# Optimization experiments

Measured on AMD Instinct MI355X. Metric: run time of the kernel, lower is better.

The kernel has to match this reference:

```python
import jax, jax.numpy as jnp
import numpy as np

EMBED_DIM = 1024
NUM_HEADS = 16
HEAD_DIM = EMBED_DIM // NUM_HEADS
SCALING = HEAD_DIM ** -0.5


def setup_inputs() -> dict:
    key = jax.random.key(0)
    ks = jax.random.split(key, 10)
    B, S, D = 2, 2048, EMBED_DIM
    lim = 1.0 / np.sqrt(D)  # torch Linear default init scale
    def lin(k):
        kw, kb = jax.random.split(k)
        W = jax.random.uniform(kw, (D, D), jnp.float32, -lim, lim)
        b = jax.random.uniform(kb, (D,), jnp.float32, -lim, lim)
        return W, b
    Wq, bq = lin(ks[0])
    Wk, bk = lin(ks[1])
    Wv, bv = lin(ks[2])
    Wo, bo = lin(ks[3])
    hidden_states = jax.random.normal(ks[4], (B, S, D), jnp.float32)
    attention_mask = jnp.ones((B, S), jnp.int32)  # unused by the module's forward
    return {"hidden_states": hidden_states, "attention_mask": attention_mask,
            "Wq": Wq, "bq": bq, "Wk": Wk, "bk": bk, "Wv": Wv, "bv": bv,
            "Wo": Wo, "bo": bo}


def reference(hidden_states, attention_mask, Wq, bq, Wk, bk, Wv, bv, Wo, bo):
    B, S, D = hidden_states.shape
    H, hd = NUM_HEADS, HEAD_DIM

    def split_heads(x):  # [B,S,D] -> [B,H,S,hd]
        return x.reshape(B, S, H, hd).transpose(0, 2, 1, 3)

    q = split_heads(hidden_states @ Wq.T + bq) * SCALING
    k = split_heads(hidden_states @ Wk.T + bk)
    v = split_heads(hidden_states @ Wv.T + bv)

    scores = jnp.einsum("bhqd,bhkd->bhqk", q, k)  # [B,H,S,S]
    mask_value = jnp.finfo(scores.dtype).min
    causal = jnp.triu(jnp.ones((S, S), bool), k=1)  # True above diagonal
    scores = jnp.where(causal, mask_value, scores)
    probs = jax.nn.softmax(scores, axis=-1)

    out = jnp.einsum("bhqk,bhkd->bhqd", probs, v)  # [B,H,S,hd]
    out = out.transpose(0, 2, 1, 3).reshape(B, S, D)
    return out @ Wo.T + bo
```

## Files before the change

### kernel.cpp

```cpp
#include <hip/hip_runtime.h>


typedef __bf16 bf16;
typedef __attribute__((ext_vector_type(8))) __bf16 bf16x8;
typedef __attribute__((ext_vector_type(4))) __bf16 bf16x4;
typedef __attribute__((ext_vector_type(4))) float f32x4;

#define MFMA16(a, b, c) __builtin_amdgcn_mfma_f32_16x16x32_bf16((a), (b), (c), 0, 0, 0)

__device__ __forceinline__ void gl_lds16(const bf16* g, bf16* l) {
  __builtin_amdgcn_global_load_lds(
      (__attribute__((address_space(1))) void*)g,
      (__attribute__((address_space(3))) void*)l, 16, 0, 0);
}

__global__ __launch_bounds__(256) void cvt5(
    const float* __restrict__ x, const float* __restrict__ wq,
    const float* __restrict__ wk, const float* __restrict__ wv,
    const float* __restrict__ wo,
    bf16* __restrict__ xb, bf16* __restrict__ wqb, bf16* __restrict__ wkb,
    bf16* __restrict__ wvb, bf16* __restrict__ wob) {
  const int bx = blockIdx.x;
  const float* s;
  bf16* d;
  int base;
  if (bx < 4096)      { s = x;  d = xb;  base = bx; }
  else if (bx < 5120) { s = wq; d = wqb; base = bx - 4096; }
  else if (bx < 6144) { s = wk; d = wkb; base = bx - 5120; }
  else if (bx < 7168) { s = wv; d = wvb; base = bx - 6144; }
  else                { s = wo; d = wob; base = bx - 7168; }
  const int i = base * 1024 + threadIdx.x * 4;
  const float4 v = *(const float4*)(s + i);
  bf16x4 o;
  o[0] = (bf16)v.x; o[1] = (bf16)v.y; o[2] = (bf16)v.z; o[3] = (bf16)v.w;
  *(bf16x4*)(d + i) = o;
}

__global__ __launch_bounds__(256) void vtrans(const bf16* __restrict__ v,
                                              bf16* __restrict__ vt) {
  __shared__ bf16 Ts[64 * 80];
  const int t = threadIdx.x;
  const int st = blockIdx.x;
  const int bh = blockIdx.y;
  const int bb = bh >> 4, h = bh & 15;
  const bf16* src = v + ((size_t)bb * 2048 + st * 64) * 1024 + h * 64;
#pragma unroll
  for (int i = 0; i < 2; ++i) {
    const int idx = i * 256 + t;
    const int sl = idx >> 3, c = idx & 7;
    *(bf16x8*)&Ts[sl * 80 + c * 8] = *(const bf16x8*)(src + (size_t)sl * 1024 + c * 8);
  }
  __syncthreads();
  bf16* dst = vt + (size_t)bh * 64 * 2048 + st * 64;
#pragma unroll
  for (int i = 0; i < 2; ++i) {
    const int idx = i * 256 + t;
    const int d = idx >> 3, c2 = idx & 7;
    bf16x8 tmp;
#pragma unroll
    for (int e = 0; e < 8; ++e) tmp[e] = Ts[(c2 * 8 + e) * 80 + d];
    *(bf16x8*)(dst + (size_t)d * 2048 + c2 * 8) = tmp;
  }
}

template <int BM, typename OutT>
__global__ __launch_bounds__(256, 2) void gemm_bt3(
    const bf16* __restrict__ A,
    const bf16* __restrict__ W0, const bf16* __restrict__ W1, const bf16* __restrict__ W2,
    const float* __restrict__ B0, const float* __restrict__ B1, const float* __restrict__ B2,
    OutT* __restrict__ O0, OutT* __restrict__ O1, OutT* __restrict__ O2,
    float s0, float s1, float s2, int K) {
  constexpr int WM = BM / 32;
  __shared__ bf16 As[BM * 64];
  __shared__ bf16 Bs[128 * 64];

  const int t = threadIdx.x;
  const int lane = t & 63;
  const int wv = t >> 6;
  const int wm = wv & 1, wn = wv >> 1;
  const int qd = lane >> 4, ln = lane & 15;

  const int which = blockIdx.x >> 3;
  const bf16* W = (which == 0) ? W0 : (which == 1) ? W1 : W2;
  const float* Bi = (which == 0) ? B0 : (which == 1) ? B1 : B2;
  OutT* O = (which == 0) ? O0 : (which == 1) ? O1 : O2;
  const float scale = (which == 0) ? s0 : (which == 1) ? s1 : s2;

  const int n0 = (blockIdx.x & 7) * 128;
  const int m0 = blockIdx.y * BM;

  f32x4 acc[WM][4] = {};

  for (int k0 = 0; k0 < K; k0 += 64) {
#pragma unroll
    for (int i = 0; i < BM / 32; ++i) {
      const int s = i * 256 + t;
      const int row = s >> 3;
      const int c = (s & 7) ^ (row & 7);
      gl_lds16(A + (size_t)(m0 + row) * K + k0 + c * 8, &As[s * 8]);
    }
#pragma unroll
    for (int i = 0; i < 4; ++i) {
      const int s = i * 256 + t;
      const int row = s >> 3;
      const int c = (s & 7) ^ (row & 7);
      gl_lds16(W + (size_t)(n0 + row) * K + k0 + c * 8, &Bs[s * 8]);
    }
    __syncthreads();

#pragma unroll
    for (int ks = 0; ks < 2; ++ks) {
      bf16x8 af[WM], bw[4];
#pragma unroll
      for (int i = 0; i < WM; ++i) {
        const int r = wm * (BM / 2) + i * 16 + ln;
        af[i] = *(const bf16x8*)&As[r * 64 + (((ks * 4 + qd) ^ (ln & 7)) << 3)];
      }
#pragma unroll
      for (int j = 0; j < 4; ++j) {
        const int r = wn * 64 + j * 16 + ln;
        bw[j] = *(const bf16x8*)&Bs[r * 64 + (((ks * 4 + qd) ^ (ln & 7)) << 3)];
      }
#pragma unroll
      for (int i = 0; i < WM; ++i)
#pragma unroll
        for (int j = 0; j < 4; ++j)
          acc[i][j] = MFMA16(af[i], bw[j], acc[i][j]);
    }
    __syncthreads();
  }

#pragma unroll
  for (int i = 0; i < WM; ++i) {
    const int row = m0 + wm * (BM / 2) + i * 16 + qd * 4;
#pragma unroll
    for (int j = 0; j < 4; ++j) {
      const int col = n0 + wn * 64 + j * 16 + ln;
      const float bias = Bi[col];
#pragma unroll
      for (int r = 0; r < 4; ++r) {
        const float v = (acc[i][j][r] + bias) * scale;
        O[(size_t)(row + r) * 1024 + col] = (OutT)v;
      }
    }
  }
}

__global__ __launch_bounds__(256, 4) void attn_causal(
    const bf16* __restrict__ Q, const bf16* __restrict__ Kg,
    const bf16* __restrict__ VT, bf16* __restrict__ Ob) {
  __shared__ bf16 Ks[2][64 * 64];
  __shared__ bf16 Vts[2][64 * 64];
  __shared__ bf16 Ps[4][16 * 64];

  const int t = threadIdx.x;
  const int lane = t & 63;
  const int w = t >> 6;
  const int qd = lane >> 4, ln = lane & 15;

  const int blk = blockIdx.x;
  const int bh = blk & 31;
  const int g = blk >> 5;
  const int a = g & 7, b = g >> 3;
  const int tq = (b == 0) ? (31 - a) : (b == 1) ? (16 + a) : (b == 2) ? (15 - a) : a;
  const int bb = bh >> 4, h = bh & 15;
  const size_t rowbase = (size_t)bb * 2048;
  const bf16* vtb = VT + (size_t)bh * 64 * 2048;

  const int q0 = tq * 64;
  const int nj = tq + 1;

  auto stage = [&](int buf, int j) {
    const bf16* kp = Kg + (rowbase + j * 64) * 1024 + h * 64;
#pragma unroll
    for (int i = 0; i < 2; ++i) {
      const int s = i * 256 + t;
      const int kv = s >> 3;
      const int c = (s & 7) ^ (kv & 7);
      gl_lds16(kp + (size_t)kv * 1024 + c * 8, &Ks[buf][s * 8]);
    }
#pragma unroll
    for (int i = 0; i < 2; ++i) {
      const int s = i * 256 + t;
      const int d = s >> 3;
      const int c = (s & 7) ^ (d & 7);
      gl_lds16(vtb + (size_t)d * 2048 + j * 64 + c * 8, &Vts[buf][s * 8]);
    }
  };

  const bf16* qp = Q + (rowbase + q0 + w * 16) * 1024 + h * 64;
  bf16x8 qf[2];
#pragma unroll
  for (int ks = 0; ks < 2; ++ks)
    qf[ks] = *(const bf16x8*)(qp + (size_t)ln * 1024 + ks * 32 + qd * 8);

  float l_run[4] = {0.f, 0.f, 0.f, 0.f};
  f32x4 accO[4] = {};

  stage(0, 0);

#pragma unroll 1
  for (int j = 0; j < nj; ++j) {
    const int buf = j & 1;
    __syncthreads();
    if (j + 1 < nj) stage(buf ^ 1, j + 1);

    f32x4 accS[4] = {};
#pragma unroll
    for (int ks = 0; ks < 2; ++ks) {
#pragma unroll
      for (int nt = 0; nt < 4; ++nt) {
        const bf16x8 bk = *(const bf16x8*)
            &Ks[buf][(nt * 16 + ln) * 64 + (((ks * 4 + qd) ^ (ln & 7)) << 3)];
        accS[nt] = MFMA16(qf[ks], bk, accS[nt]);
      }
    }

    if (j == nj - 1) {
#pragma unroll
      for (int r = 0; r < 4; ++r) {
        const int row = qd * 4 + r;
        const int qg = q0 + w * 16 + row;
        float sum = 0.f;
#pragma unroll
        for (int nt = 0; nt < 4; ++nt) {
          float p = __expf(accS[nt][r]);
          const int col = nt * 16 + ln;
          if ((j * 64 + col) > qg) p = 0.f;
          sum += p;
          Ps[w][row * 64 + ((((col >> 3) ^ (row & 7))) << 3) + (col & 7)] = (bf16)p;
        }
        l_run[r] += sum;
      }
    } else {
#pragma unroll
      for (int r = 0; r < 4; ++r) {
        const int row = qd * 4 + r;
        float sum = 0.f;
#pragma unroll
        for (int nt = 0; nt < 4; ++nt) {
          const float p = __expf(accS[nt][r]);
          const int col = nt * 16 + ln;
          sum += p;
          Ps[w][row * 64 + ((((col >> 3) ^ (row & 7))) << 3) + (col & 7)] = (bf16)p;
        }
        l_run[r] += sum;
      }
    }

#pragma unroll
    for (int kt = 0; kt < 2; ++kt) {
      const bf16x8 ap = *(const bf16x8*)
          &Ps[w][ln * 64 + (((kt * 4 + qd) ^ (ln & 7)) << 3)];
#pragma unroll
      for (int nt = 0; nt < 4; ++nt) {
        const bf16x8 bv = *(const bf16x8*)
            &Vts[buf][(nt * 16 + ln) * 64 + (((kt * 4 + qd) ^ (ln & 7)) << 3)];
        accO[nt] = MFMA16(ap, bv, accO[nt]);
      }
    }
  }

  bf16* op = Ob + (rowbase + q0 + w * 16) * 1024 + h * 64;
#pragma unroll
  for (int r = 0; r < 4; ++r) {
    float l = l_run[r];
#pragma unroll
    for (int off = 1; off < 16; off <<= 1) l += __shfl_xor(l, off, 64);
    const float inv_l = 1.0f / l;
#pragma unroll
    for (int nt = 0; nt < 4; ++nt)
      op[(size_t)(qd * 4 + r) * 1024 + nt * 16 + ln] = (bf16)(accO[nt][r] * inv_l);
  }
}

extern "C" void kernel_launch(void* const* d_in, const int* in_sizes, int n_in,
                              void* d_out, int out_size, void* d_ws, size_t ws_size,
                              hipStream_t stream) {
  const float* X  = (const float*)d_in[0];
  const float* Wq = (const float*)d_in[2];
  const float* bq = (const float*)d_in[3];
  const float* Wk = (const float*)d_in[4];
  const float* bk = (const float*)d_in[5];
  const float* Wv = (const float*)d_in[6];
  const float* bv = (const float*)d_in[7];
  const float* Wo = (const float*)d_in[8];
  const float* bo = (const float*)d_in[9];
  float* out = (float*)d_out;

  bf16* xb  = (bf16*)d_ws;
  bf16* wqb = xb  + (size_t)4096 * 1024;
  bf16* wkb = wqb + (size_t)1024 * 1024;
  bf16* wvb = wkb + (size_t)1024 * 1024;
  bf16* wob = wvb + (size_t)1024 * 1024;
  bf16* q   = wob + (size_t)1024 * 1024;
  bf16* k   = q   + (size_t)4096 * 1024;
  bf16* v   = k   + (size_t)4096 * 1024;
  bf16* vt  = v   + (size_t)4096 * 1024;
  bf16* ao  = xb;

  const float scaling = 0.125f;

  dim3 blk(256);
  cvt5<<<dim3(8192), blk, 0, stream>>>(X, Wq, Wk, Wv, Wo, xb, wqb, wkb, wvb, wob);
  gemm_bt3<128, bf16><<<dim3(24, 32), blk, 0, stream>>>(
      xb, wqb, wkb, wvb, bq, bk, bv, q, k, v, scaling, 1.f, 1.f, 1024);
  vtrans<<<dim3(32, 32), blk, 0, stream>>>(v, vt);
  attn_causal<<<dim3(1024), blk, 0, stream>>>(q, k, vt, ao);
  gemm_bt3<64, float><<<dim3(8, 64), blk, 0, stream>>>(
      ao, wob, wob, wob, bo, bo, bo, out, out, out, 1.f, 1.f, 1.f, 1024);
}
```

Before: 183.2 us.

## Double attention query tile per block to reuse K/V tiles across 128 rows

Each attention block now handles 128 query rows, with each wave owning 32 rows as two 16-row MFMA tiles, so every staged K/V tile feeds twice as many MMAs. The grid is halved, the block-to-tile schedule is simplified, and the causal mask is applied on the last two KV tiles. The log2(e) factor is folded into the Q scaling so exp2 can replace expf. This raises register pressure (launch bounds drop from 4 to 2 blocks per CU) and halves the block count, which may hurt occupancy and load balance.

After: 197.6 us. +7.8%, slower.

```diff
diff --git a/kernel.cpp b/kernel.cpp
--- a/kernel.cpp
+++ b/kernel.cpp
@@ -146,12 +146,12 @@
   }
 }
 
-__global__ __launch_bounds__(256, 4) void attn_causal(
+__global__ __launch_bounds__(256, 2) void attn_causal(
     const bf16* __restrict__ Q, const bf16* __restrict__ Kg,
     const bf16* __restrict__ VT, bf16* __restrict__ Ob) {
   __shared__ bf16 Ks[2][64 * 64];
   __shared__ bf16 Vts[2][64 * 64];
-  __shared__ bf16 Ps[4][16 * 64];
+  __shared__ bf16 Ps[4][32 * 64];
 
   const int t = threadIdx.x;
   const int lane = t & 63;
@@ -161,14 +161,13 @@
   const int blk = blockIdx.x;
   const int bh = blk & 31;
   const int g = blk >> 5;
-  const int a = g & 7, b = g >> 3;
-  const int tq = (b == 0) ? (31 - a) : (b == 1) ? (16 + a) : (b == 2) ? (15 - a) : a;
+  const int tq = (g < 8) ? (15 - g) : (g - 8);
   const int bb = bh >> 4, h = bh & 15;
   const size_t rowbase = (size_t)bb * 2048;
   const bf16* vtb = VT + (size_t)bh * 64 * 2048;
 
-  const int q0 = tq * 64;
-  const int nj = tq + 1;
+  const int q0 = tq * 128;
+  const int nj = 2 * tq + 2;
 
   auto stage = [&](int buf, int j) {
     const bf16* kp = Kg + (rowbase + j * 64) * 1024 + h * 64;
@@ -188,14 +187,16 @@
     }
   };
 
-  const bf16* qp = Q + (rowbase + q0 + w * 16) * 1024 + h * 64;
-  bf16x8 qf[2];
-#pragma unroll
-  for (int ks = 0; ks < 2; ++ks)
-    qf[ks] = *(const bf16x8*)(qp + (size_t)ln * 1024 + ks * 32 + qd * 8);
-
-  float l_run[4] = {0.f, 0.f, 0.f, 0.f};
-  f32x4 accO[4] = {};
+  const bf16* qp = Q + (rowbase + q0 + w * 32) * 1024 + h * 64;
+  bf16x8 qf[2][2];
+#pragma unroll
+  for (int m = 0; m < 2; ++m)
+#pragma unroll
+    for (int ks = 0; ks < 2; ++ks)
+      qf[m][ks] = *(const bf16x8*)(qp + (size_t)(m * 16 + ln) * 1024 + ks * 32 + qd * 8);
+
+  float l_run[2][4] = {};
+  f32x4 accO[2][4] = {};
 
   stage(0, 0);
 
@@ -205,72 +206,87 @@
     __syncthreads();
     if (j + 1 < nj) stage(buf ^ 1, j + 1);
 
-    f32x4 accS[4] = {};
+    f32x4 accS[2][4] = {};
 #pragma unroll
     for (int ks = 0; ks < 2; ++ks) {
 #pragma unroll
       for (int nt = 0; nt < 4; ++nt) {
         const bf16x8 bk = *(const bf16x8*)
             &Ks[buf][(nt * 16 + ln) * 64 + (((ks * 4 + qd) ^ (ln & 7)) << 3)];
-        accS[nt] = MFMA16(qf[ks], bk, accS[nt]);
-      }
-    }
-
-    if (j == nj - 1) {
-#pragma unroll
-      for (int r = 0; r < 4; ++r) {
-        const int row = qd * 4 + r;
-        const int qg = q0 + w * 16 + row;
-        float sum = 0.f;
-#pragma unroll
-        for (int nt = 0; nt < 4; ++nt) {
-          float p = __expf(accS[nt][r]);
-          const int col = nt * 16 + ln;
-          if ((j * 64 + col) > qg) p = 0.f;
-          sum += p;
-          Ps[w][row * 64 + ((((col >> 3) ^ (row & 7))) << 3) + (col & 7)] = (bf16)p;
+#pragma unroll
+        for (int m = 0; m < 2; ++m)
+          accS[m][nt] = MFMA16(qf[m][ks], bk, accS[m][nt]);
+      }
+    }
+
+    if (j >= nj - 2) {
+#pragma unroll
+      for (int m = 0; m < 2; ++m)
+#pragma unroll
+        for (int r = 0; r < 4; ++r) {
+          const int row = m * 16 + qd * 4 + r;
+          const int qg = q0 + w * 32 + row;
+          float sum = 0.f;
+#pragma unroll
+          for (int nt = 0; nt < 4; ++nt) {
+            float p = __builtin_exp2f(accS[m][nt][r]);
+            const int col = nt * 16 + ln;
+            if ((j * 64 + col) > qg) p = 0.f;
+            sum += p;
+            Ps[w][row * 64 + ((((col >> 3) ^ (row & 7))) << 3) + (col & 7)] = (bf16)p;
+          }
+          l_run[m][r] += sum;
         }
-        l_run[r] += sum;
-      }
     } else {
 #pragma unroll
-      for (int r = 0; r < 4; ++r) {
-        const int row = qd * 4 + r;
-        float sum = 0.f;
-#pragma unroll
-        for (int nt = 0; nt < 4; ++nt) {
-          const float p = __expf(accS[nt][r]);
-          const int col = nt * 16 + ln;
-          sum += p;
-          Ps[w][row * 64 + ((((col >> 3) ^ (row & 7))) << 3) + (col & 7)] = (bf16)p;
+      for (int m = 0; m < 2; ++m)
+#pragma unroll
+        for (int r = 0; r < 4; ++r) {
+          const int row = m * 16 + qd * 4 + r;
+          float sum = 0.f;
+#pragma unroll
+          for (int nt = 0; nt < 4; ++nt) {
+            const float p = __builtin_exp2f(accS[m][nt][r]);
+            const int col = nt * 16 + ln;
+            sum += p;
+            Ps[w][row * 64 + ((((col >> 3) ^ (row & 7))) << 3) + (col & 7)] = (bf16)p;
+          }
+          l_run[m][r] += sum;
         }
-        l_run[r] += sum;
-      }
     }
 
 #pragma unroll
     for (int kt = 0; kt < 2; ++kt) {
-      const bf16x8 ap = *(const bf16x8*)
-          &Ps[w][ln * 64 + (((kt * 4 + qd) ^ (ln & 7)) << 3)];
+      bf16x8 ap[2];
+#pragma unroll
+      for (int m = 0; m < 2; ++m)
+        ap[m] = *(const bf16x8*)
+            &Ps[w][(m * 16 + ln) * 64 + (((kt * 4 + qd) ^ (ln & 7)) << 3)];
 #pragma unroll
       for (int nt = 0; nt < 4; ++nt) {
         const bf16x8 bv = *(const bf16x8*)
             &Vts[buf][(nt * 16 + ln) * 64 + (((kt * 4 + qd) ^ (ln & 7)) << 3)];
-        accO[nt] = MFMA16(ap, bv, accO[nt]);
-      }
-    }
-  }
-
-  bf16* op = Ob + (rowbase + q0 + w * 16) * 1024 + h * 64;
-#pragma unroll
-  for (int r = 0; r < 4; ++r) {
-    float l = l_run[r];
-#pragma unroll
-    for (int off = 1; off < 16; off <<= 1) l += __shfl_xor(l, off, 64);
-    const float inv_l = 1.0f / l;
-#pragma unroll
-    for (int nt = 0; nt < 4; ++nt)
-      op[(size_t)(qd * 4 + r) * 1024 + nt * 16 + ln] = (bf16)(accO[nt][r] * inv_l);
+#pragma unroll
+        for (int m = 0; m < 2; ++m)
+          accO[m][nt] = MFMA16(ap[m], bv, accO[m][nt]);
+      }
+    }
+  }
+
+  bf16* op = Ob + (rowbase + q0 + w * 32) * 1024 + h * 64;
+#pragma unroll
+  for (int m = 0; m < 2; ++m) {
+#pragma unroll
+    for (int r = 0; r < 4; ++r) {
+      float l = l_run[m][r];
+#pragma unroll
+      for (int off = 1; off < 16; off <<= 1) l += __shfl_xor(l, off, 64);
+      const float inv_l = 1.0f / l;
+#pragma unroll
+      for (int nt = 0; nt < 4; ++nt)
+        op[(size_t)(m * 16 + qd * 4 + r) * 1024 + nt * 16 + ln] =
+            (bf16)(accO[m][nt][r] * inv_l);
+    }
   }
 }
 
@@ -299,14 +315,14 @@
   bf16* vt  = v   + (size_t)4096 * 1024;
   bf16* ao  = xb;
 
-  const float scaling = 0.125f;
+  const float scaling = 0.125f * 1.44269504088896f;
 
   dim3 blk(256);
   cvt5<<<dim3(8192), blk, 0, stream>>>(X, Wq, Wk, Wv, Wo, xb, wqb, wkb, wvb, wob);
   gemm_bt3<128, bf16><<<dim3(24, 32), blk, 0, stream>>>(
       xb, wqb, wkb, wvb, bq, bk, bv, q, k, v, scaling, 1.f, 1.f, 1024);
   vtrans<<<dim3(32, 32), blk, 0, stream>>>(v, vt);
-  attn_causal<<<dim3(1024), blk, 0, stream>>>(q, k, vt, ao);
+  attn_causal<<<dim3(512), blk, 0, stream>>>(q, k, vt, ao);
   gemm_bt3<64, float><<<dim3(8, 64), blk, 0, stream>>>(
       ao, wob, wob, wob, bo, bo, bo, out, out, out, 1.f, 1.f, 1.f, 1024);
 }
```

## Fuse V transpose into QKV GEMM epilogue and use exp2 with folded log2e

Applied to the files above, without the earlier changes.

The QKV projection epilogue now writes the V output directly in transposed [B,H,hd,S] layout, which removes the separate vtrans kernel and its extra read and write of V. The Q scaling factor also folds in log2(e), so the attention softmax can use exp2 instead of __expf. The transposed stores are 4-element bf16 vectors strided by 2048, which may coalesce less well than the row-major writes. Folding log2(e) into Q changes the rounding of the bf16 Q values slightly.

After: 189.4 us. 3.4% more time.

```diff
diff --git a/kernel.cpp b/kernel.cpp
--- a/kernel.cpp
+++ b/kernel.cpp
@@ -36,40 +36,13 @@
   *(bf16x4*)(d + i) = o;
 }
 
-__global__ __launch_bounds__(256) void vtrans(const bf16* __restrict__ v,
-                                              bf16* __restrict__ vt) {
-  __shared__ bf16 Ts[64 * 80];
-  const int t = threadIdx.x;
-  const int st = blockIdx.x;
-  const int bh = blockIdx.y;
-  const int bb = bh >> 4, h = bh & 15;
-  const bf16* src = v + ((size_t)bb * 2048 + st * 64) * 1024 + h * 64;
-#pragma unroll
-  for (int i = 0; i < 2; ++i) {
-    const int idx = i * 256 + t;
-    const int sl = idx >> 3, c = idx & 7;
-    *(bf16x8*)&Ts[sl * 80 + c * 8] = *(const bf16x8*)(src + (size_t)sl * 1024 + c * 8);
-  }
-  __syncthreads();
-  bf16* dst = vt + (size_t)bh * 64 * 2048 + st * 64;
-#pragma unroll
-  for (int i = 0; i < 2; ++i) {
-    const int idx = i * 256 + t;
-    const int d = idx >> 3, c2 = idx & 7;
-    bf16x8 tmp;
-#pragma unroll
-    for (int e = 0; e < 8; ++e) tmp[e] = Ts[(c2 * 8 + e) * 80 + d];
-    *(bf16x8*)(dst + (size_t)d * 2048 + c2 * 8) = tmp;
-  }
-}
-
 template <int BM, typename OutT>
 __global__ __launch_bounds__(256, 2) void gemm_bt3(
     const bf16* __restrict__ A,
     const bf16* __restrict__ W0, const bf16* __restrict__ W1, const bf16* __restrict__ W2,
     const float* __restrict__ B0, const float* __restrict__ B1, const float* __restrict__ B2,
     OutT* __restrict__ O0, OutT* __restrict__ O1, OutT* __restrict__ O2,
-    float s0, float s1, float s2, int K) {
+    float s0, float s1, float s2, int K, int vt_which) {
   constexpr int WM = BM / 32;
   __shared__ bf16 As[BM * 64];
   __shared__ bf16 Bs[128 * 64];
@@ -137,10 +110,25 @@
     for (int j = 0; j < 4; ++j) {
       const int col = n0 + wn * 64 + j * 16 + ln;
       const float bias = Bi[col];
-#pragma unroll
-      for (int r = 0; r < 4; ++r) {
-        const float v = (acc[i][j][r] + bias) * scale;
-        O[(size_t)(row + r) * 1024 + col] = (OutT)v;
+      if (which == vt_which) {
+        const int bb = row >> 11, ss = row & 2047;
+        const int hh = col >> 6, dd = col & 63;
+        OutT* dst = O + ((size_t)((bb << 4) + hh) * 64 + dd) * 2048 + ss;
+        if constexpr (sizeof(OutT) == 2) {
+          bf16x4 pk;
+#pragma unroll
+          for (int r = 0; r < 4; ++r) pk[r] = (bf16)((acc[i][j][r] + bias) * scale);
+          *(bf16x4*)dst = pk;
+        } else {
+#pragma unroll
+          for (int r = 0; r < 4; ++r) dst[r] = (OutT)((acc[i][j][r] + bias) * scale);
+        }
+      } else {
+#pragma unroll
+        for (int r = 0; r < 4; ++r) {
+          const float v = (acc[i][j][r] + bias) * scale;
+          O[(size_t)(row + r) * 1024 + col] = (OutT)v;
+        }
       }
     }
   }
@@ -224,7 +212,7 @@
         float sum = 0.f;
 #pragma unroll
         for (int nt = 0; nt < 4; ++nt) {
-          float p = __expf(accS[nt][r]);
+          float p = __builtin_exp2f(accS[nt][r]);
           const int col = nt * 16 + ln;
           if ((j * 64 + col) > qg) p = 0.f;
           sum += p;
@@ -239,7 +227,7 @@
         float sum = 0.f;
 #pragma unroll
         for (int nt = 0; nt < 4; ++nt) {
-          const float p = __expf(accS[nt][r]);
+          const float p = __builtin_exp2f(accS[nt][r]);
           const int col = nt * 16 + ln;
           sum += p;
           Ps[w][row * 64 + ((((col >> 3) ^ (row & 7))) << 3) + (col & 7)] = (bf16)p;
@@ -295,18 +283,16 @@
   bf16* wob = wvb + (size_t)1024 * 1024;
   bf16* q   = wob + (size_t)1024 * 1024;
   bf16* k   = q   + (size_t)4096 * 1024;
-  bf16* v   = k   + (size_t)4096 * 1024;
-  bf16* vt  = v   + (size_t)4096 * 1024;
+  bf16* vt  = k   + (size_t)4096 * 1024;
   bf16* ao  = xb;
 
-  const float scaling = 0.125f;
+  const float scaling = 0.125f * 1.44269504088896f;
 
   dim3 blk(256);
   cvt5<<<dim3(8192), blk, 0, stream>>>(X, Wq, Wk, Wv, Wo, xb, wqb, wkb, wvb, wob);
   gemm_bt3<128, bf16><<<dim3(24, 32), blk, 0, stream>>>(
-      xb, wqb, wkb, wvb, bq, bk, bv, q, k, v, scaling, 1.f, 1.f, 1024);
-  vtrans<<<dim3(32, 32), blk, 0, stream>>>(v, vt);
+      xb, wqb, wkb, wvb, bq, bk, bv, q, k, vt, scaling, 1.f, 1.f, 1024, 2);
   attn_causal<<<dim3(1024), blk, 0, stream>>>(q, k, vt, ao);
   gemm_bt3<64, float><<<dim3(8, 64), blk, 0, stream>>>(
-      ao, wob, wob, wob, bo, bo, bo, out, out, out, 1.f, 1.f, 1.f, 1024);
-}
+      ao, wob, wob, wob, bo, bo, bo, out, out, out, 1.f, 1.f, 1.f, 1024, -1);
+}
```
